# Kernel tuning notes

Hardware: AMD Instinct MI355X
Metric: run time of the kernel (lower is better)

Reference implementation:

```python
import jax, jax.numpy as jnp
import numpy as np

B, T, L, D = 4, 32, 64, 768
NHEAD, DFF, NLAYERS, NSPK = 12, 2048, 2, 4
DH = D // NHEAD


def setup_inputs() -> dict:
    key = jax.random.key(0)
    ks = jax.random.split(key, 12)
    s = 0.02
    return {
        "token_embeddings": jax.random.normal(ks[0], (B, T, L, D), jnp.float32) * s,
        "speaker_ids": jax.random.randint(ks[1], (B, T), 0, NSPK, jnp.int32),
        "Wq": jax.random.normal(ks[2], (D, D), jnp.float32) * s,
        "Wk": jax.random.normal(ks[3], (D, D), jnp.float32) * s,
        "Wv": jax.random.normal(ks[4], (D, D), jnp.float32) * s,
        "in_proj_w": jax.random.normal(ks[5], (NLAYERS, 3 * D, D), jnp.float32) * s,
        "in_proj_b": jnp.zeros((NLAYERS, 3 * D), jnp.float32),
        "out_w": jax.random.normal(ks[6], (NLAYERS, D, D), jnp.float32) * s,
        "out_b": jnp.zeros((NLAYERS, D), jnp.float32),
        "ln1_g": jnp.ones((NLAYERS, D), jnp.float32),
        "ln1_b": jnp.zeros((NLAYERS, D), jnp.float32),
        "ff1_w": jax.random.normal(ks[7], (NLAYERS, DFF, D), jnp.float32) * s,
        "ff1_b": jnp.zeros((NLAYERS, DFF), jnp.float32),
        "ff2_w": jax.random.normal(ks[8], (NLAYERS, D, DFF), jnp.float32) * s,
        "ff2_b": jnp.zeros((NLAYERS, D), jnp.float32),
        "ln2_g": jnp.ones((NLAYERS, D), jnp.float32),
        "ln2_b": jnp.zeros((NLAYERS, D), jnp.float32),
    }


def _layer_norm(x, g, b, eps=1e-5):
    mu = x.mean(-1, keepdims=True)
    var = ((x - mu) ** 2).mean(-1, keepdims=True)
    return (x - mu) * jax.lax.rsqrt(var + eps) * g + b


def _mha(x, w_in, b_in, w_out, b_out):
    # x: (N, L, D); torch nn.MultiheadAttention with in_proj/out_proj
    N, Lx, _ = x.shape
    qkv = x @ w_in.T + b_in  # (N, L, 3D)
    q, k, v = jnp.split(qkv, 3, axis=-1)
    def heads(z):
        return z.reshape(N, Lx, NHEAD, DH).transpose(0, 2, 1, 3)  # (N,H,L,dh)
    q, k, v = heads(q), heads(k), heads(v)
    scores = jnp.einsum("nhqd,nhkd->nhqk", q, k) / jnp.sqrt(jnp.float32(DH))
    attn = jax.nn.softmax(scores, axis=-1)
    out = jnp.einsum("nhqk,nhkd->nhqd", attn, v)
    out = out.transpose(0, 2, 1, 3).reshape(N, Lx, D)
    return out @ w_out.T + b_out


def reference(token_embeddings, speaker_ids, Wq, Wk, Wv, in_proj_w, in_proj_b,
              out_w, out_b, ln1_g, ln1_b, ff1_w, ff1_b, ff2_w, ff2_b, ln2_g, ln2_b):
    # edu embeddings: mean over token dim (frozen-BERT output stand-in)
    edu = token_embeddings.mean(axis=2)              # (B,T,D)
    tok = token_embeddings @ Wq.T                    # query_proj on tokens (B,T,L,D)
    k = edu @ Wk.T                                   # (B,T,D)
    v = edu @ Wv.T                                   # (B,T,D)
    # SAUTE: per-speaker causal cumulative sum of outer products k_u v_u^T
    same_spk = speaker_ids[:, :, None] == speaker_ids[:, None, :]
    causal = jnp.arange(T)[None, :, None] >= jnp.arange(T)[None, None, :]
    maskf = (same_spk & causal).astype(k.dtype)      # (B,T,T)
    M = jnp.einsum("btu,bui,buj->btij", maskf, k, v)  # (B,T,D,D) speaker state
    ctx = tok + jnp.einsum("btij,btlj->btli", M, tok)  # (B,T,L,D)
    # stacked post-norm TransformerEncoder (torch defaults: ReLU, dff=2048)
    x = ctx.reshape(B * T, L, D)
    for l in range(NLAYERS):
        a = _mha(x, in_proj_w[l], in_proj_b[l], out_w[l], out_b[l])
        x = _layer_norm(x + a, ln1_g[l], ln1_b[l])
        f = jax.nn.relu(x @ ff1_w[l].T + ff1_b[l]) @ ff2_w[l].T + ff2_b[l]
        x = _layer_norm(x + f, ln2_g[l], ln2_b[l])
    return x.reshape(B, T, L, D)
```

## Files before the change

kernel.cpp:

```cpp
#include <hip/hip_runtime.h>
#include <hip/hip_bf16.h>

#define BB 4
#define TT 32
#define LL 64
#define DD 768
#define NHEAD 12
#define DH 64
#define DFF 2048
#define NLAYERS 2
#define ROWS (BB*TT*LL)
#define BTN  (BB*TT)

typedef __attribute__((ext_vector_type(8))) short bf16x8;
typedef __attribute__((ext_vector_type(4))) float f32x4;

__device__ __forceinline__ int swz(int r, int c) {
    return r * 32 + ((c ^ ((r >> 1) & 3)) << 3);
}

__device__ __forceinline__ int xcd_swizzle(int orig, int nwg) {
    const int q8 = nwg >> 3, r8 = nwg & 7;
    const int xcd = orig & 7, idx = orig >> 3;
    return (xcd < r8 ? xcd * (q8 + 1) : r8 * (q8 + 1) + (xcd - r8) * q8) + idx;
}

__device__ __forceinline__ unsigned pack_bf16(float a, float b) {
    __hip_bfloat16 h0 = __float2bfloat16(a);
    __hip_bfloat16 h1 = __float2bfloat16(b);
    return (unsigned)*reinterpret_cast<unsigned short*>(&h0) |
           ((unsigned)*reinterpret_cast<unsigned short*>(&h1) << 16);
}

__device__ __forceinline__ short bf16s(float a) {
    __hip_bfloat16 h = __float2bfloat16(a);
    return *reinterpret_cast<short*>(&h);
}

struct CastArgs {
    const float* src[7];
    __hip_bfloat16* dst[7];
    int end[7];
};
__global__ __launch_bounds__(256) void cast_multi_kernel(CastArgs a)
{
    int q = blockIdx.x * 256 + threadIdx.x;
    if (q >= a.end[6]) return;
    int s = 0;
    while (q >= a.end[s]) ++s;
    int local = q - (s ? a.end[s - 1] : 0);
    float4 v = reinterpret_cast<const float4*>(a.src[s])[local];
    ushort4 o;
    __hip_bfloat16 h0 = __float2bfloat16(v.x);
    __hip_bfloat16 h1 = __float2bfloat16(v.y);
    __hip_bfloat16 h2 = __float2bfloat16(v.z);
    __hip_bfloat16 h3 = __float2bfloat16(v.w);
    o.x = *reinterpret_cast<unsigned short*>(&h0);
    o.y = *reinterpret_cast<unsigned short*>(&h1);
    o.z = *reinterpret_cast<unsigned short*>(&h2);
    o.w = *reinterpret_cast<unsigned short*>(&h3);
    reinterpret_cast<ushort4*>(a.dst[s])[local] = o;
}

__global__ __launch_bounds__(256) void te_prep_kernel(
    const float* __restrict__ te, __hip_bfloat16* __restrict__ teb,
    __hip_bfloat16* __restrict__ edu_b)
{
    int idx = blockIdx.x * 256 + threadIdx.x;
    int bt = idx / DD;
    int d  = idx - bt * DD;
    const float* p = te + ((size_t)bt * LL) * DD + d;
    __hip_bfloat16* q = teb + ((size_t)bt * LL) * DD + d;
    float s = 0.f;
#pragma unroll
    for (int l = 0; l < LL; ++l) {
        float v = p[(size_t)l * DD];
        s += v;
        q[(size_t)l * DD] = __float2bfloat16(v);
    }
    edu_b[idx] = __float2bfloat16(s * (1.0f / (float)LL));
}

template<int OUT_BF16, int RELU, int QKV>
__global__ __launch_bounds__(256) void gemm_bf16_kernel(
    const __hip_bfloat16* __restrict__ A,
    const __hip_bfloat16* __restrict__ B,
    const float* __restrict__ bias,
    void* __restrict__ Cout,
    __hip_bfloat16* __restrict__ Vout,
    int M, int N, int K, int ldC)
{
    __shared__ short lA[2][4096];
    __shared__ short lB[2][4096];
    const int tid  = threadIdx.x;
    const int lane = tid & 63;
    const int w    = tid >> 6;
    const int wr   = w >> 1, wc = w & 1;

    const int nbx = gridDim.x;
    const int wg = xcd_swizzle(blockIdx.y * nbx + blockIdx.x, nbx * gridDim.y);
    const int bm = (wg / nbx) * 128;
    const int bn = (wg % nbx) * 128;

    const int sr  = tid >> 2;
    const int cw  = tid & 3;
    const int sco = cw << 3;

    const int wo0 = swz(sr, cw);
    const int wo1 = swz(sr + 64, cw);
    int roA[4], roB[4];
#pragma unroll
    for (int m = 0; m < 4; ++m)
        roA[m] = swz(wr * 64 + m * 16 + (lane & 15), lane >> 4);
#pragma unroll
    for (int n = 0; n < 4; ++n)
        roB[n] = swz(wc * 64 + n * 16 + (lane & 15), lane >> 4);

    const short* Ag = reinterpret_cast<const short*>(A);
    const short* Bg = reinterpret_cast<const short*>(B);

    f32x4 acc[4][4] = {};

    bf16x8 ra0 = *reinterpret_cast<const bf16x8*>(Ag + (size_t)(bm + sr) * K + sco);
    bf16x8 ra1 = *reinterpret_cast<const bf16x8*>(Ag + (size_t)(bm + 64 + sr) * K + sco);
    bf16x8 rb0 = *reinterpret_cast<const bf16x8*>(Bg + (size_t)(bn + sr) * K + sco);
    bf16x8 rb1 = *reinterpret_cast<const bf16x8*>(Bg + (size_t)(bn + 64 + sr) * K + sco);
    *reinterpret_cast<bf16x8*>(&lA[0][wo0]) = ra0;
    *reinterpret_cast<bf16x8*>(&lA[0][wo1]) = ra1;
    *reinterpret_cast<bf16x8*>(&lB[0][wo0]) = rb0;
    *reinterpret_cast<bf16x8*>(&lB[0][wo1]) = rb1;
    __syncthreads();

    const int NT = K >> 5;
    int cur = 0;
    for (int t = 0; t < NT; ++t) {
        const bool nx = (t + 1 < NT);
        if (nx) {
            const int kn = (t + 1) << 5;
            ra0 = *reinterpret_cast<const bf16x8*>(Ag + (size_t)(bm + sr) * K + kn + sco);
            ra1 = *reinterpret_cast<const bf16x8*>(Ag + (size_t)(bm + 64 + sr) * K + kn + sco);
            rb0 = *reinterpret_cast<const bf16x8*>(Bg + (size_t)(bn + sr) * K + kn + sco);
            rb1 = *reinterpret_cast<const bf16x8*>(Bg + (size_t)(bn + 64 + sr) * K + kn + sco);
        }

        bf16x8 af[4], bfr[4];
#pragma unroll
        for (int m = 0; m < 4; ++m)
            af[m] = *reinterpret_cast<const bf16x8*>(&lA[cur][roA[m]]);
#pragma unroll
        for (int n = 0; n < 4; ++n)
            bfr[n] = *reinterpret_cast<const bf16x8*>(&lB[cur][roB[n]]);
#pragma unroll
        for (int m = 0; m < 4; ++m)
#pragma unroll
            for (int n = 0; n < 4; ++n)
                acc[m][n] = __builtin_amdgcn_mfma_f32_16x16x32_bf16(
                    af[m], bfr[n], acc[m][n], 0, 0, 0);

        if (nx) {
            *reinterpret_cast<bf16x8*>(&lA[cur ^ 1][wo0]) = ra0;
            *reinterpret_cast<bf16x8*>(&lA[cur ^ 1][wo1]) = ra1;
            *reinterpret_cast<bf16x8*>(&lB[cur ^ 1][wo0]) = rb0;
            *reinterpret_cast<bf16x8*>(&lB[cur ^ 1][wo1]) = rb1;
        }
        __syncthreads();
        cur ^= 1;
    }

    const int crow = (lane >> 4) * 4;
    const int ccol = lane & 15;
#pragma unroll
    for (int n = 0; n < 4; ++n) {
        const int col = bn + wc * 64 + n * 16 + ccol;
        const float bv = bias ? bias[col] : 0.f;
        if (QKV && col >= 1536) {
            const int hh = (col - 1536) >> 6;
            const int d  = (col - 1536) & 63;
#pragma unroll
            for (int m = 0; m < 4; ++m) {
                const int row0 = bm + wr * 64 + m * 16 + crow;
#pragma unroll
                for (int j = 0; j < 4; ++j) {
                    const int row = row0 + j;
                    const int ni = row >> 6, ll = row & 63;
                    Vout[(((size_t)ni * NHEAD + hh) << 12) + (d << 6) + ll] =
                        __float2bfloat16(acc[m][n][j] + bv);
                }
            }
        } else {
#pragma unroll
            for (int m = 0; m < 4; ++m) {
                const int row0 = bm + wr * 64 + m * 16 + crow;
#pragma unroll
                for (int j = 0; j < 4; ++j) {
                    float v = acc[m][n][j] + bv;
                    if (RELU) v = fmaxf(v, 0.f);
                    if (OUT_BF16)
                        reinterpret_cast<__hip_bfloat16*>(Cout)[(size_t)(row0 + j) * ldC + col] =
                            __float2bfloat16(v);
                    else
                        reinterpret_cast<float*>(Cout)[(size_t)(row0 + j) * ldC + col] = v;
                }
            }
        }
    }
}

__global__ __launch_bounds__(64) void attn_mfma_kernel(
    const __hip_bfloat16* __restrict__ qk,
    const __hip_bfloat16* __restrict__ vt,
    __hip_bfloat16* __restrict__ out)
{
    const int n = blockIdx.x, h = blockIdx.y;
    const int lane = threadIdx.x;
    const int lo = lane & 15, hi = lane >> 4;
    __shared__ short pl[64 * 72];

    const short* qg = reinterpret_cast<const short*>(qk) + (size_t)(n * 64) * 1536 + h * 64;

    f32x4 acc[4][4] = {};
#pragma unroll
    for (int ks = 0; ks < 2; ++ks) {
        const int kc = ks * 32 + hi * 8;
        bf16x8 af[4], bk[4];
#pragma unroll
        for (int m = 0; m < 4; ++m)
            af[m] = *reinterpret_cast<const bf16x8*>(qg + (size_t)(m * 16 + lo) * 1536 + kc);
#pragma unroll
        for (int nn = 0; nn < 4; ++nn)
            bk[nn] = *reinterpret_cast<const bf16x8*>(qg + 768 + (size_t)(nn * 16 + lo) * 1536 + kc);
#pragma unroll
        for (int m = 0; m < 4; ++m)
#pragma unroll
            for (int nn = 0; nn < 4; ++nn)
                acc[m][nn] = __builtin_amdgcn_mfma_f32_16x16x32_bf16(
                    af[m], bk[nn], acc[m][nn], 0, 0, 0);
    }

#pragma unroll
    for (int m = 0; m < 4; ++m) {
#pragma unroll
        for (int j = 0; j < 4; ++j) {
            float s0 = acc[m][0][j] * 0.125f;
            float s1 = acc[m][1][j] * 0.125f;
            float s2 = acc[m][2][j] * 0.125f;
            float s3 = acc[m][3][j] * 0.125f;
            float mx = fmaxf(fmaxf(s0, s1), fmaxf(s2, s3));
            mx = fmaxf(mx, __shfl_xor(mx, 1));
            mx = fmaxf(mx, __shfl_xor(mx, 2));
            mx = fmaxf(mx, __shfl_xor(mx, 4));
            mx = fmaxf(mx, __shfl_xor(mx, 8));
            float e0 = __expf(s0 - mx), e1 = __expf(s1 - mx);
            float e2 = __expf(s2 - mx), e3 = __expf(s3 - mx);
            float sm = e0 + e1 + e2 + e3;
            sm += __shfl_xor(sm, 1);
            sm += __shfl_xor(sm, 2);
            sm += __shfl_xor(sm, 4);
            sm += __shfl_xor(sm, 8);
            const float inv = 1.0f / sm;
            short* pr = &pl[(m * 16 + hi * 4 + j) * 72 + lo];
            pr[0]  = bf16s(e0 * inv);
            pr[16] = bf16s(e1 * inv);
            pr[32] = bf16s(e2 * inv);
            pr[48] = bf16s(e3 * inv);
        }
    }
    __syncthreads();

    const short* vg = reinterpret_cast<const short*>(vt) + ((size_t)(n * NHEAD + h) << 12);
    f32x4 o[4][4] = {};
#pragma unroll
    for (int ks = 0; ks < 2; ++ks) {
        const int kc = ks * 32 + hi * 8;
        bf16x8 pa[4], bv[4];
#pragma unroll
        for (int m = 0; m < 4; ++m)
            pa[m] = *reinterpret_cast<const bf16x8*>(&pl[(m * 16 + lo) * 72 + kc]);
#pragma unroll
        for (int nn = 0; nn < 4; ++nn)
            bv[nn] = *reinterpret_cast<const bf16x8*>(vg + (nn * 16 + lo) * 64 + kc);
#pragma unroll
        for (int m = 0; m < 4; ++m)
#pragma unroll
            for (int nn = 0; nn < 4; ++nn)
                o[m][nn] = __builtin_amdgcn_mfma_f32_16x16x32_bf16(
                    pa[m], bv[nn], o[m][nn], 0, 0, 0);
    }

#pragma unroll
    for (int m = 0; m < 4; ++m)
#pragma unroll
        for (int nn = 0; nn < 4; ++nn)
#pragma unroll
            for (int j = 0; j < 4; ++j)
                out[(size_t)(n * 64 + m * 16 + hi * 4 + j) * DD + h * 64 + nn * 16 + lo] =
                    __float2bfloat16(o[m][nn][j]);
}

__global__ __launch_bounds__(64) void saute_p_mfma_kernel(
    const __hip_bfloat16* __restrict__ Xb,
    const __hip_bfloat16* __restrict__ KV,
    const int* __restrict__ spk,
    __hip_bfloat16* __restrict__ P)
{
    const int lane = threadIdx.x;
    const int lo = lane & 15, hi = lane >> 4;
    const int row0 = blockIdx.x * 64;
    const int bt = row0 >> 6;
    const int b  = bt >> 5, t = bt & 31;

    const short* Ag = reinterpret_cast<const short*>(Xb) + (size_t)row0 * DD;
    const short* Bg = reinterpret_cast<const short*>(KV) + (size_t)(b * TT) * 1536 + 768;

    f32x4 acc[4][2] = {};
    for (int ks = 0; ks < 24; ++ks) {
        const int kc = ks * 32 + hi * 8;
        bf16x8 af[4], bv[2];
#pragma unroll
        for (int m = 0; m < 4; ++m)
            af[m] = *reinterpret_cast<const bf16x8*>(Ag + (size_t)(m * 16 + lo) * DD + kc);
#pragma unroll
        for (int nn = 0; nn < 2; ++nn)
            bv[nn] = *reinterpret_cast<const bf16x8*>(Bg + (size_t)(nn * 16 + lo) * 1536 + kc);
#pragma unroll
        for (int m = 0; m < 4; ++m)
#pragma unroll
            for (int nn = 0; nn < 2; ++nn)
                acc[m][nn] = __builtin_amdgcn_mfma_f32_16x16x32_bf16(
                    af[m], bv[nn], acc[m][nn], 0, 0, 0);
    }

    const int st = spk[bt];
#pragma unroll
    for (int nn = 0; nn < 2; ++nn) {
        const int u = nn * 16 + lo;
        const bool mk = (u <= t) && (spk[b * TT + u] == st);
#pragma unroll
        for (int m = 0; m < 4; ++m)
#pragma unroll
            for (int j = 0; j < 4; ++j) {
                const int row = row0 + m * 16 + hi * 4 + j;
                P[(size_t)row * 32 + u] =
                    mk ? __float2bfloat16(acc[m][nn][j]) : __float2bfloat16(0.f);
            }
    }
}

__global__ __launch_bounds__(256) void saute_ctx_kernel(
    __hip_bfloat16* __restrict__ Xb,
    const __hip_bfloat16* __restrict__ KV,
    const __hip_bfloat16* __restrict__ P)
{
    __shared__ unsigned kls[32 * 384];
    __shared__ float pls[8 * 32];
    const int row0 = blockIdx.x * 8;
    const int b = row0 >> 11;
    const int tid = threadIdx.x;

    const unsigned* k2 = reinterpret_cast<const unsigned*>(KV) + (size_t)(b * TT) * 768;
    for (int i = tid; i < 32 * 384; i += 256) {
        int u = i / 384, j = i - u * 384;
        kls[i] = k2[u * 768 + j];
    }
    pls[tid] = __bfloat162float(P[(size_t)row0 * 32 + tid]);
    __syncthreads();

    const int r = tid >> 5;
    const int l32 = tid & 31;
    unsigned* xrow = reinterpret_cast<unsigned*>(Xb + (size_t)(row0 + r) * DD);

    float2 acc[12];
#pragma unroll
    for (int c = 0; c < 12; ++c) {
        unsigned pk = xrow[l32 + 32 * c];
        acc[c].x = __uint_as_float(pk << 16);
        acc[c].y = __uint_as_float(pk & 0xffff0000u);
    }
    for (int u = 0; u < 32; ++u) {
        const float pv = pls[r * 32 + u];
        const unsigned* kr = &kls[u * 384];
#pragma unroll
        for (int c = 0; c < 12; ++c) {
            unsigned pk = kr[l32 + 32 * c];
            acc[c].x = fmaf(pv, __uint_as_float(pk << 16),          acc[c].x);
            acc[c].y = fmaf(pv, __uint_as_float(pk & 0xffff0000u), acc[c].y);
        }
    }
#pragma unroll
    for (int c = 0; c < 12; ++c)
        xrow[l32 + 32 * c] = pack_bf16(acc[c].x, acc[c].y);
}

template<int FINAL>
__global__ __launch_bounds__(192) void add_ln_kernel(
    __hip_bfloat16* __restrict__ xb, const __hip_bfloat16* __restrict__ y,
    const float* __restrict__ g, const float* __restrict__ bb,
    float* __restrict__ xf)
{
    const int row = blockIdx.x;
    const int tid = threadIdx.x;
    __shared__ float red[3];
    __shared__ float stat[2];
    const size_t base = (size_t)row * DD + tid * 4;

    uint2 xv = *reinterpret_cast<const uint2*>(xb + base);
    uint2 yv = *reinterpret_cast<const uint2*>(y + base);
    float v[4];
    v[0] = __uint_as_float(xv.x << 16)         + __uint_as_float(yv.x << 16);
    v[1] = __uint_as_float(xv.x & 0xffff0000u) + __uint_as_float(yv.x & 0xffff0000u);
    v[2] = __uint_as_float(xv.y << 16)         + __uint_as_float(yv.y << 16);
    v[3] = __uint_as_float(xv.y & 0xffff0000u) + __uint_as_float(yv.y & 0xffff0000u);

    float s = v[0] + v[1] + v[2] + v[3];
#pragma unroll
    for (int off = 32; off > 0; off >>= 1) s += __shfl_down(s, off);
    if ((tid & 63) == 0) red[tid >> 6] = s;
    __syncthreads();
    if (tid == 0) stat[0] = (red[0] + red[1] + red[2]) * (1.0f / (float)DD);
    __syncthreads();
    const float mu = stat[0];

    float d[4];
    float q = 0.f;
#pragma unroll
    for (int i = 0; i < 4; ++i) { d[i] = v[i] - mu; q += d[i] * d[i]; }
    __syncthreads();
#pragma unroll
    for (int off = 32; off > 0; off >>= 1) q += __shfl_down(q, off);
    if ((tid & 63) == 0) red[tid >> 6] = q;
    __syncthreads();
    if (tid == 0) stat[1] = (red[0] + red[1] + red[2]) * (1.0f / (float)DD);
    __syncthreads();
    const float rstd = rsqrtf(stat[1] + 1e-5f);

    float o[4];
#pragma unroll
    for (int i = 0; i < 4; ++i)
        o[i] = d[i] * rstd * g[tid * 4 + i] + bb[tid * 4 + i];

    if (FINAL) {
        float4 f4 = make_float4(o[0], o[1], o[2], o[3]);
        *reinterpret_cast<float4*>(xf + base) = f4;
    } else {
        uint2 ov;
        ov.x = pack_bf16(o[0], o[1]);
        ov.y = pack_bf16(o[2], o[3]);
        *reinterpret_cast<uint2*>(xb + base) = ov;
    }
}

extern "C" void kernel_launch(void* const* d_in, const int* in_sizes, int n_in,
                              void* d_out, int out_size, void* d_ws, size_t ws_size,
                              hipStream_t stream) {
    (void)in_sizes; (void)n_in; (void)out_size; (void)ws_size;
    const float* te  = (const float*)d_in[0];
    const int*   spk = (const int*)  d_in[1];
    const float* Wq  = (const float*)d_in[2];
    const float* Wk  = (const float*)d_in[3];
    const float* Wv  = (const float*)d_in[4];
    const float* ipw = (const float*)d_in[5];
    const float* ipb = (const float*)d_in[6];
    const float* ow  = (const float*)d_in[7];
    const float* ob  = (const float*)d_in[8];
    const float* g1  = (const float*)d_in[9];
    const float* b1  = (const float*)d_in[10];
    const float* f1w = (const float*)d_in[11];
    const float* f1b = (const float*)d_in[12];
    const float* f2w = (const float*)d_in[13];
    const float* f2b = (const float*)d_in[14];
    const float* g2  = (const float*)d_in[15];
    const float* b2  = (const float*)d_in[16];

    float* Xout = (float*)d_out;

    __hip_bfloat16* wsb   = (__hip_bfloat16*)d_ws;
    __hip_bfloat16* Wq_b  = wsb;
    __hip_bfloat16* ipw_b = Wq_b  + 589824;
    __hip_bfloat16* ow_b  = ipw_b + 3538944;
    __hip_bfloat16* f1w_b = ow_b  + 1179648;
    __hip_bfloat16* f2w_b = f1w_b + 3145728;
    __hip_bfloat16* Xb    = f2w_b + 3145728;
    __hip_bfloat16* SCR   = Xb    + 6291456;
    __hip_bfloat16* Vt    = SCR   + 12582912;
    __hip_bfloat16* Wkv_b = SCR;
    __hip_bfloat16* Ab    = SCR   + 18874368;
    __hip_bfloat16* Yb    = Ab    + 6291456;
    __hip_bfloat16* KV    = Yb    + 6291456;
    __hip_bfloat16* Pb    = KV    + 196608;
    __hip_bfloat16* edu_b = Pb    + 262144;

    te_prep_kernel<<<(BTN * DD) / 256, 256, 0, stream>>>(te, Ab, edu_b);

    CastArgs ca;
    ca.src[0] = Wq;  ca.dst[0] = Wq_b;
    ca.src[1] = ipw; ca.dst[1] = ipw_b;
    ca.src[2] = ow;  ca.dst[2] = ow_b;
    ca.src[3] = f1w; ca.dst[3] = f1w_b;
    ca.src[4] = f2w; ca.dst[4] = f2w_b;
    ca.src[5] = Wk;  ca.dst[5] = Wkv_b;
    ca.src[6] = Wv;  ca.dst[6] = Wkv_b + 589824;
    int quads[7] = {589824/4, 3538944/4, 1179648/4, 3145728/4, 3145728/4, 589824/4, 589824/4};
    int acc = 0;
    for (int i = 0; i < 7; ++i) { acc += quads[i]; ca.end[i] = acc; }
    cast_multi_kernel<<<(acc + 255) / 256, 256, 0, stream>>>(ca);

    gemm_bf16_kernel<1,0,0><<<dim3(1536/128, 1), 256, 0, stream>>>(
        edu_b, Wkv_b, nullptr, KV, nullptr, BTN, 1536, DD, 1536);

    gemm_bf16_kernel<1,0,0><<<dim3(DD/128, ROWS/128), 256, 0, stream>>>(
        Ab, Wq_b, nullptr, Xb, nullptr, ROWS, DD, DD, DD);

    saute_p_mfma_kernel<<<ROWS/64, 64, 0, stream>>>(Xb, KV, spk, Pb);
    saute_ctx_kernel<<<ROWS/8, 256, 0, stream>>>(Xb, KV, Pb);

    for (int l = 0; l < NLAYERS; ++l) {
        const __hip_bfloat16* ipw_l = ipw_b + (size_t)l * 3 * DD * DD;
        const __hip_bfloat16* ow_l  = ow_b  + (size_t)l * DD * DD;
        const __hip_bfloat16* f1w_l = f1w_b + (size_t)l * DFF * DD;
        const __hip_bfloat16* f2w_l = f2w_b + (size_t)l * DD * DFF;

        gemm_bf16_kernel<1,0,1><<<dim3(3*DD/128, ROWS/128), 256, 0, stream>>>(
            Xb, ipw_l, ipb + (size_t)l * 3 * DD, SCR, Vt, ROWS, 3*DD, DD, 1536);
        attn_mfma_kernel<<<dim3(BTN, NHEAD), 64, 0, stream>>>(SCR, Vt, Ab);
        gemm_bf16_kernel<1,0,0><<<dim3(DD/128, ROWS/128), 256, 0, stream>>>(
            Ab, ow_l, ob + (size_t)l * DD, Yb, nullptr, ROWS, DD, DD, DD);
        add_ln_kernel<0><<<ROWS, 192, 0, stream>>>(
            Xb, Yb, g1 + (size_t)l * DD, b1 + (size_t)l * DD, nullptr);
        gemm_bf16_kernel<1,1,0><<<dim3(DFF/128, ROWS/128), 256, 0, stream>>>(
            Xb, f1w_l, f1b + (size_t)l * DFF, SCR, nullptr, ROWS, DFF, DD, DFF);
        gemm_bf16_kernel<1,0,0><<<dim3(DD/128, ROWS/128), 256, 0, stream>>>(
            SCR, f2w_l, f2b + (size_t)l * DD, Yb, nullptr, ROWS, DD, DFF, DD);
        if (l == NLAYERS - 1)
            add_ln_kernel<1><<<ROWS, 192, 0, stream>>>(
                Xb, Yb, g2 + (size_t)l * DD, b2 + (size_t)l * DD, Xout);
        else
            add_ln_kernel<0><<<ROWS, 192, 0, stream>>>(
                Xb, Yb, g2 + (size_t)l * DD, b2 + (size_t)l * DD, nullptr);
    }
}
```

Measured before the change: 457.1 us.

## Load GEMM tiles directly into LDS with global_load_lds, single-buffered

The GEMM kernel now fetches A and B tiles straight from global memory into LDS using the buffer-to-LDS builtin, replacing register staging and the double-buffered LDS prefetch. LDS use is halved and there are fewer VGPRs, which may raise occupancy. The cost is that global loads no longer overlap with the MFMA work inside a block, because each k-step loads and then syncs. The template parameters also become runtime flags, which adds branches in the epilogue.

Result: slower. 521.5 us (+14.1%).

```diff
diff --git a/kernel.cpp b/kernel.cpp
--- a/kernel.cpp
+++ b/kernel.cpp
@@ -14,6 +14,10 @@
 
 typedef __attribute__((ext_vector_type(8))) short bf16x8;
 typedef __attribute__((ext_vector_type(4))) float f32x4;
+
+#define GLOAD_LDS16(g, l) __builtin_amdgcn_global_load_lds( \
+    (const __attribute__((address_space(1))) void*)(g),     \
+    (__attribute__((address_space(3))) void*)(l), 16, 0, 0)
 
 __device__ __forceinline__ int swz(int r, int c) {
     return r * 32 + ((c ^ ((r >> 1) & 3)) << 3);
@@ -81,17 +85,16 @@
     edu_b[idx] = __float2bfloat16(s * (1.0f / (float)LL));
 }
 
-template<int OUT_BF16, int RELU, int QKV>
 __global__ __launch_bounds__(256) void gemm_bf16_kernel(
     const __hip_bfloat16* __restrict__ A,
     const __hip_bfloat16* __restrict__ B,
     const float* __restrict__ bias,
     void* __restrict__ Cout,
     __hip_bfloat16* __restrict__ Vout,
-    int M, int N, int K, int ldC)
-{
-    __shared__ short lA[2][4096];
-    __shared__ short lB[2][4096];
+    int M, int N, int K, int ldC, int flags)
+{
+    __shared__ short lA[4096];
+    __shared__ short lB[4096];
     const int tid  = threadIdx.x;
     const int lane = tid & 63;
     const int w    = tid >> 6;
@@ -102,12 +105,16 @@
     const int bm = (wg / nbx) * 128;
     const int bn = (wg % nbx) * 128;
 
-    const int sr  = tid >> 2;
-    const int cw  = tid & 3;
-    const int sco = cw << 3;
-
-    const int wo0 = swz(sr, cw);
-    const int wo1 = swz(sr + 64, cw);
+    const int sr0 = (w * 2) * 16 + (lane >> 2);
+    const int sr1 = (w * 2 + 1) * 16 + (lane >> 2);
+    const int cwl = lane & 3;
+    const int sc0 = (cwl ^ ((sr0 >> 1) & 3)) << 3;
+    const int sc1 = (cwl ^ ((sr1 >> 1) & 3)) << 3;
+    short* dstA0 = &lA[(w * 2) * 512];
+    short* dstA1 = &lA[(w * 2 + 1) * 512];
+    short* dstB0 = &lB[(w * 2) * 512];
+    short* dstB1 = &lB[(w * 2 + 1) * 512];
+
     int roA[4], roB[4];
 #pragma unroll
     for (int m = 0; m < 4; ++m)
@@ -121,50 +128,29 @@
 
     f32x4 acc[4][4] = {};
 
-    bf16x8 ra0 = *reinterpret_cast<const bf16x8*>(Ag + (size_t)(bm + sr) * K + sco);
-    bf16x8 ra1 = *reinterpret_cast<const bf16x8*>(Ag + (size_t)(bm + 64 + sr) * K + sco);
-    bf16x8 rb0 = *reinterpret_cast<const bf16x8*>(Bg + (size_t)(bn + sr) * K + sco);
-    bf16x8 rb1 = *reinterpret_cast<const bf16x8*>(Bg + (size_t)(bn + 64 + sr) * K + sco);
-    *reinterpret_cast<bf16x8*>(&lA[0][wo0]) = ra0;
-    *reinterpret_cast<bf16x8*>(&lA[0][wo1]) = ra1;
-    *reinterpret_cast<bf16x8*>(&lB[0][wo0]) = rb0;
-    *reinterpret_cast<bf16x8*>(&lB[0][wo1]) = rb1;
-    __syncthreads();
-
     const int NT = K >> 5;
-    int cur = 0;
     for (int t = 0; t < NT; ++t) {
-        const bool nx = (t + 1 < NT);
-        if (nx) {
-            const int kn = (t + 1) << 5;
-            ra0 = *reinterpret_cast<const bf16x8*>(Ag + (size_t)(bm + sr) * K + kn + sco);
-            ra1 = *reinterpret_cast<const bf16x8*>(Ag + (size_t)(bm + 64 + sr) * K + kn + sco);
-            rb0 = *reinterpret_cast<const bf16x8*>(Bg + (size_t)(bn + sr) * K + kn + sco);
-            rb1 = *reinterpret_cast<const bf16x8*>(Bg + (size_t)(bn + 64 + sr) * K + kn + sco);
-        }
+        const int k0 = t << 5;
+        GLOAD_LDS16(Ag + (size_t)(bm + sr0) * K + k0 + sc0, dstA0);
+        GLOAD_LDS16(Ag + (size_t)(bm + sr1) * K + k0 + sc1, dstA1);
+        GLOAD_LDS16(Bg + (size_t)(bn + sr0) * K + k0 + sc0, dstB0);
+        GLOAD_LDS16(Bg + (size_t)(bn + sr1) * K + k0 + sc1, dstB1);
+        __syncthreads();
 
         bf16x8 af[4], bfr[4];
 #pragma unroll
         for (int m = 0; m < 4; ++m)
-            af[m] = *reinterpret_cast<const bf16x8*>(&lA[cur][roA[m]]);
+            af[m] = *reinterpret_cast<const bf16x8*>(&lA[roA[m]]);
 #pragma unroll
         for (int n = 0; n < 4; ++n)
-            bfr[n] = *reinterpret_cast<const bf16x8*>(&lB[cur][roB[n]]);
+            bfr[n] = *reinterpret_cast<const bf16x8*>(&lB[roB[n]]);
 #pragma unroll
         for (int m = 0; m < 4; ++m)
 #pragma unroll
             for (int n = 0; n < 4; ++n)
                 acc[m][n] = __builtin_amdgcn_mfma_f32_16x16x32_bf16(
                     af[m], bfr[n], acc[m][n], 0, 0, 0);
-
-        if (nx) {
-            *reinterpret_cast<bf16x8*>(&lA[cur ^ 1][wo0]) = ra0;
-            *reinterpret_cast<bf16x8*>(&lA[cur ^ 1][wo1]) = ra1;
-            *reinterpret_cast<bf16x8*>(&lB[cur ^ 1][wo0]) = rb0;
-            *reinterpret_cast<bf16x8*>(&lB[cur ^ 1][wo1]) = rb1;
-        }
         __syncthreads();
-        cur ^= 1;
     }
 
     const int crow = (lane >> 4) * 4;
@@ -173,7 +159,7 @@
     for (int n = 0; n < 4; ++n) {
         const int col = bn + wc * 64 + n * 16 + ccol;
         const float bv = bias ? bias[col] : 0.f;
-        if (QKV && col >= 1536) {
+        if ((flags & 4) && col >= 1536) {
             const int hh = (col - 1536) >> 6;
             const int d  = (col - 1536) & 63;
 #pragma unroll
@@ -194,8 +180,8 @@
 #pragma unroll
                 for (int j = 0; j < 4; ++j) {
                     float v = acc[m][n][j] + bv;
-                    if (RELU) v = fmaxf(v, 0.f);
-                    if (OUT_BF16)
+                    if (flags & 2) v = fmaxf(v, 0.f);
+                    if (flags & 1)
                         reinterpret_cast<__hip_bfloat16*>(Cout)[(size_t)(row0 + j) * ldC + col] =
                             __float2bfloat16(v);
                     else
@@ -504,11 +490,11 @@
     for (int i = 0; i < 7; ++i) { acc += quads[i]; ca.end[i] = acc; }
     cast_multi_kernel<<<(acc + 255) / 256, 256, 0, stream>>>(ca);
 
-    gemm_bf16_kernel<1,0,0><<<dim3(1536/128, 1), 256, 0, stream>>>(
-        edu_b, Wkv_b, nullptr, KV, nullptr, BTN, 1536, DD, 1536);
-
-    gemm_bf16_kernel<1,0,0><<<dim3(DD/128, ROWS/128), 256, 0, stream>>>(
-        Ab, Wq_b, nullptr, Xb, nullptr, ROWS, DD, DD, DD);
+    gemm_bf16_kernel<<<dim3(1536/128, 1), 256, 0, stream>>>(
+        edu_b, Wkv_b, nullptr, KV, nullptr, BTN, 1536, DD, 1536, 1);
+
+    gemm_bf16_kernel<<<dim3(DD/128, ROWS/128), 256, 0, stream>>>(
+        Ab, Wq_b, nullptr, Xb, nullptr, ROWS, DD, DD, DD, 1);
 
     saute_p_mfma_kernel<<<ROWS/64, 64, 0, stream>>>(Xb, KV, spk, Pb);
     saute_ctx_kernel<<<ROWS/8, 256, 0, stream>>>(Xb, KV, Pb);
@@ -519,17 +505,17 @@
         const __hip_bfloat16* f1w_l = f1w_b + (size_t)l * DFF * DD;
         const __hip_bfloat16* f2w_l = f2w_b + (size_t)l * DD * DFF;
 
-        gemm_bf16_kernel<1,0,1><<<dim3(3*DD/128, ROWS/128), 256, 0, stream>>>(
-            Xb, ipw_l, ipb + (size_t)l * 3 * DD, SCR, Vt, ROWS, 3*DD, DD, 1536);
+        gemm_bf16_kernel<<<dim3(3*DD/128, ROWS/128), 256, 0, stream>>>(
+            Xb, ipw_l, ipb + (size_t)l * 3 * DD, SCR, Vt, ROWS, 3*DD, DD, 1536, 1 | 4);
         attn_mfma_kernel<<<dim3(BTN, NHEAD), 64, 0, stream>>>(SCR, Vt, Ab);
-        gemm_bf16_kernel<1,0,0><<<dim3(DD/128, ROWS/128), 256, 0, stream>>>(
-            Ab, ow_l, ob + (size_t)l * DD, Yb, nullptr, ROWS, DD, DD, DD);
+        gemm_bf16_kernel<<<dim3(DD/128, ROWS/128), 256, 0, stream>>>(
+            Ab, ow_l, ob + (size_t)l * DD, Yb, nullptr, ROWS, DD, DD, DD, 1);
         add_ln_kernel<0><<<ROWS, 192, 0, stream>>>(
             Xb, Yb, g1 + (size_t)l * DD, b1 + (size_t)l * DD, nullptr);
-        gemm_bf16_kernel<1,1,0><<<dim3(DFF/128, ROWS/128), 256, 0, stream>>>(
-            Xb, f1w_l, f1b + (size_t)l * DFF, SCR, nullptr, ROWS, DFF, DD, DFF);
-        gemm_bf16_kernel<1,0,0><<<dim3(DD/128, ROWS/128), 256, 0, stream>>>(
-            SCR, f2w_l, f2b + (size_t)l * DD, Yb, nullptr, ROWS, DD, DFF, DD);
+        gemm_bf16_kernel<<<dim3(DFF/128, ROWS/128), 256, 0, stream>>>(
+            Xb, f1w_l, f1b + (size_t)l * DFF, SCR, nullptr, ROWS, DFF, DD, DFF, 1 | 2);
+        gemm_bf16_kernel<<<dim3(DD/128, ROWS/128), 256, 0, stream>>>(
+            SCR, f2w_l, f2b + (size_t)l * DD, Yb, nullptr, ROWS, DD, DFF, DD, 1);
         if (l == NLAYERS - 1)
             add_ln_kernel<1><<<ROWS, 192, 0, stream>>>(
                 Xb, Yb, g2 + (size_t)l * DD, b2 + (size_t)l * DD, Xout);
```

## Add 256x128-tile GEMM with direct global-to-LDS loads for QKV and FF1

Applied to the files above, without the earlier changes.

Adds a new GEMM kernel with a 256x128 output tile (8x4 MFMA fragments per wave) that loads A and B tiles straight into LDS via global_load_lds. The QKV projection and the first feed-forward GEMM use it instead of the 128x128 register-staged kernel. The larger tile raises data reuse per block and halves the block count. The new kernel is single-buffered with two barriers per k-step, so load latency is no longer overlapped with compute, and the larger accumulator raises register pressure.

Measured after the change: 604.1 us. +32.2%, slower.

```diff
diff --git a/kernel.cpp b/kernel.cpp
--- a/kernel.cpp
+++ b/kernel.cpp
@@ -14,6 +14,10 @@
 
 typedef __attribute__((ext_vector_type(8))) short bf16x8;
 typedef __attribute__((ext_vector_type(4))) float f32x4;
+
+#define GLOAD_LDS16(g, l) __builtin_amdgcn_global_load_lds( \
+    (const __attribute__((address_space(1))) void*)(g),     \
+    (__attribute__((address_space(3))) void*)(l), 16, 0, 0)
 
 __device__ __forceinline__ int swz(int r, int c) {
     return r * 32 + ((c ^ ((r >> 1) & 3)) << 3);
@@ -173,12 +177,115 @@
     for (int n = 0; n < 4; ++n) {
         const int col = bn + wc * 64 + n * 16 + ccol;
         const float bv = bias ? bias[col] : 0.f;
-        if (QKV && col >= 1536) {
+#pragma unroll
+        for (int m = 0; m < 4; ++m) {
+            const int row0 = bm + wr * 64 + m * 16 + crow;
+#pragma unroll
+            for (int j = 0; j < 4; ++j) {
+                float v = acc[m][n][j] + bv;
+                if (RELU) v = fmaxf(v, 0.f);
+                if (OUT_BF16)
+                    reinterpret_cast<__hip_bfloat16*>(Cout)[(size_t)(row0 + j) * ldC + col] =
+                        __float2bfloat16(v);
+                else
+                    reinterpret_cast<float*>(Cout)[(size_t)(row0 + j) * ldC + col] = v;
+            }
+        }
+    }
+}
+
+__global__ __launch_bounds__(256) void gemm_256_kernel(
+    const __hip_bfloat16* __restrict__ A,
+    const __hip_bfloat16* __restrict__ B,
+    const float* __restrict__ bias,
+    __hip_bfloat16* __restrict__ Cout,
+    __hip_bfloat16* __restrict__ Vout,
+    int M, int N, int K, int ldC, int flags)
+{
+    __shared__ short lA[8192];
+    __shared__ short lB[4096];
+    const int tid  = threadIdx.x;
+    const int lane = tid & 63;
+    const int w    = tid >> 6;
+    const int wr   = w >> 1, wc = w & 1;
+
+    const int nbx = gridDim.x;
+    const int wg = xcd_swizzle(blockIdx.y * nbx + blockIdx.x, nbx * gridDim.y);
+    const int bm = (wg / nbx) * 256;
+    const int bn = (wg % nbx) * 128;
+
+    const int lrow = lane >> 2;
+    const int lchk = lane & 3;
+    int rowA[4], scA[4];
+    short* dstA[4];
+#pragma unroll
+    for (int i = 0; i < 4; ++i) {
+        const int seg = w * 4 + i;
+        rowA[i] = seg * 16 + lrow;
+        scA[i]  = (lchk ^ ((rowA[i] >> 1) & 3)) << 3;
+        dstA[i] = &lA[seg * 512];
+    }
+    int rowB[2], scB[2];
+    short* dstB[2];
+#pragma unroll
+    for (int i = 0; i < 2; ++i) {
+        const int seg = w * 2 + i;
+        rowB[i] = seg * 16 + lrow;
+        scB[i]  = (lchk ^ ((rowB[i] >> 1) & 3)) << 3;
+        dstB[i] = &lB[seg * 512];
+    }
+
+    int roA[8], roB[4];
+#pragma unroll
+    for (int m = 0; m < 8; ++m)
+        roA[m] = swz(wr * 128 + m * 16 + (lane & 15), lane >> 4);
+#pragma unroll
+    for (int n = 0; n < 4; ++n)
+        roB[n] = swz(wc * 64 + n * 16 + (lane & 15), lane >> 4);
+
+    const short* Ag = reinterpret_cast<const short*>(A);
+    const short* Bg = reinterpret_cast<const short*>(B);
+
+    f32x4 acc[8][4] = {};
+
+    const int NT = K >> 5;
+    for (int t = 0; t < NT; ++t) {
+        const int k0 = t << 5;
+#pragma unroll
+        for (int i = 0; i < 4; ++i)
+            GLOAD_LDS16(Ag + (size_t)(bm + rowA[i]) * K + k0 + scA[i], dstA[i]);
+#pragma unroll
+        for (int i = 0; i < 2; ++i)
+            GLOAD_LDS16(Bg + (size_t)(bn + rowB[i]) * K + k0 + scB[i], dstB[i]);
+        __syncthreads();
+
+        bf16x8 bfr[4];
+#pragma unroll
+        for (int n = 0; n < 4; ++n)
+            bfr[n] = *reinterpret_cast<const bf16x8*>(&lB[roB[n]]);
+#pragma unroll
+        for (int m = 0; m < 8; ++m) {
+            bf16x8 af = *reinterpret_cast<const bf16x8*>(&lA[roA[m]]);
+#pragma unroll
+            for (int n = 0; n < 4; ++n)
+                acc[m][n] = __builtin_amdgcn_mfma_f32_16x16x32_bf16(
+                    af, bfr[n], acc[m][n], 0, 0, 0);
+        }
+        __syncthreads();
+    }
+
+    const int crow = (lane >> 4) * 4;
+    const int ccol = lane & 15;
+#pragma unroll
+    for (int n = 0; n < 4; ++n) {
+        const int col = bn + wc * 64 + n * 16 + ccol;
+        const float bv = bias ? bias[col] : 0.f;
+        if ((flags & 4) && col >= 1536) {
             const int hh = (col - 1536) >> 6;
             const int d  = (col - 1536) & 63;
 #pragma unroll
-            for (int m = 0; m < 4; ++m) {
-                const int row0 = bm + wr * 64 + m * 16 + crow;
+            for (int m = 0; m < 8; ++m) {
+                const int row0 = bm + wr * 128 + m * 16 + crow;
 #pragma unroll
                 for (int j = 0; j < 4; ++j) {
                     const int row = row0 + j;
@@ -189,17 +296,13 @@
             }
         } else {
 #pragma unroll
-            for (int m = 0; m < 4; ++m) {
-                const int row0 = bm + wr * 64 + m * 16 + crow;
+            for (int m = 0; m < 8; ++m) {
+                const int row0 = bm + wr * 128 + m * 16 + crow;
 #pragma unroll
                 for (int j = 0; j < 4; ++j) {
                     float v = acc[m][n][j] + bv;
-                    if (RELU) v = fmaxf(v, 0.f);
-                    if (OUT_BF16)
-                        reinterpret_cast<__hip_bfloat16*>(Cout)[(size_t)(row0 + j) * ldC + col] =
-                            __float2bfloat16(v);
-                    else
-                        reinterpret_cast<float*>(Cout)[(size_t)(row0 + j) * ldC + col] = v;
+                    if (flags & 2) v = fmaxf(v, 0.f);
+                    Cout[(size_t)(row0 + j) * ldC + col] = __float2bfloat16(v);
                 }
             }
         }
@@ -519,15 +622,15 @@
         const __hip_bfloat16* f1w_l = f1w_b + (size_t)l * DFF * DD;
         const __hip_bfloat16* f2w_l = f2w_b + (size_t)l * DD * DFF;
 
-        gemm_bf16_kernel<1,0,1><<<dim3(3*DD/128, ROWS/128), 256, 0, stream>>>(
-            Xb, ipw_l, ipb + (size_t)l * 3 * DD, SCR, Vt, ROWS, 3*DD, DD, 1536);
+        gemm_256_kernel<<<dim3(3*DD/128, ROWS/256), 256, 0, stream>>>(
+            Xb, ipw_l, ipb + (size_t)l * 3 * DD, SCR, Vt, ROWS, 3*DD, DD, 1536, 4);
         attn_mfma_kernel<<<dim3(BTN, NHEAD), 64, 0, stream>>>(SCR, Vt, Ab);
         gemm_bf16_kernel<1,0,0><<<dim3(DD/128, ROWS/128), 256, 0, stream>>>(
             Ab, ow_l, ob + (size_t)l * DD, Yb, nullptr, ROWS, DD, DD, DD);
         add_ln_kernel<0><<<ROWS, 192, 0, stream>>>(
             Xb, Yb, g1 + (size_t)l * DD, b1 + (size_t)l * DD, nullptr);
-        gemm_bf16_kernel<1,1,0><<<dim3(DFF/128, ROWS/128), 256, 0, stream>>>(
-            Xb, f1w_l, f1b + (size_t)l * DFF, SCR, nullptr, ROWS, DFF, DD, DFF);
+        gemm_256_kernel<<<dim3(DFF/128, ROWS/256), 256, 0, stream>>>(
+            Xb, f1w_l, f1b + (size_t)l * DFF, SCR, nullptr, ROWS, DFF, DD, DFF, 2);
         gemm_bf16_kernel<1,0,0><<<dim3(DD/128, ROWS/128), 256, 0, stream>>>(
             SCR, f2w_l, f2b + (size_t)l * DD, Yb, nullptr, ROWS, DD, DFF, DD);
         if (l == NLAYERS - 1)
```
